# Performance work log

Measured on AMD Instinct MI355X. Metric: run time of the kernel, lower is better.

Reference implementation:

```python
import jax, jax.numpy as jnp
import numpy as np

B, S, D = 4, 2048, 768
H, R = 12, 8
Dh = D // H


def setup_inputs() -> dict:
    key = jax.random.key(0)
    ks = jax.random.split(key, 12)
    s_in = 1.0 / np.sqrt(D)
    s_r = 1.0 / np.sqrt(R)
    return {
        "x": jax.random.normal(ks[0], (B, S, D), jnp.float32),
        "Wq0": jax.random.normal(ks[1], (D, D), jnp.float32) * s_in,
        "Aq": jax.random.normal(ks[2], (D, R), jnp.float32) * s_in,
        "Bq": jax.random.normal(ks[3], (R, D), jnp.float32) * s_r,
        "Wk0": jax.random.normal(ks[4], (D, D), jnp.float32) * s_in,
        "Ak": jax.random.normal(ks[5], (D, R), jnp.float32) * s_in,
        "Bk": jax.random.normal(ks[6], (R, D), jnp.float32) * s_r,
        "Wv0": jax.random.normal(ks[7], (D, D), jnp.float32) * s_in,
        "Av": jax.random.normal(ks[8], (D, R), jnp.float32) * s_in,
        "Bv": jax.random.normal(ks[9], (R, D), jnp.float32) * s_r,
        "Wo": jax.random.normal(ks[10], (D, D), jnp.float32) * s_in,
        "bo": jnp.zeros((D,), jnp.float32),
    }


def _lora(x, W0, A, Bm):
    # x @ W0 + (x @ A) @ B  -- low-rank adapter on frozen W0
    return x @ W0 + (x @ A) @ Bm


def _split_heads(t):
    # [B,S,D] -> [B,H,S,Dh]
    return t.reshape(B, S, H, Dh).transpose(0, 2, 1, 3)


def reference(x, Wq0, Aq, Bq, Wk0, Ak, Bk, Wv0, Av, Bv, Wo, bo):
    q = _split_heads(_lora(x, Wq0, Aq, Bq))
    k = _split_heads(_lora(x, Wk0, Ak, Bk))
    v = _split_heads(_lora(x, Wv0, Av, Bv))
    scale = 1.0 / jnp.sqrt(jnp.asarray(Dh, x.dtype))
    scores = jnp.einsum("bhqd,bhkd->bhqk", q, k) * scale  # [B,H,S,S]
    weights = jax.nn.softmax(scores, axis=-1)
    attn = jnp.einsum("bhqk,bhkd->bhqd", weights, v)
    concat = attn.transpose(0, 2, 1, 3).reshape(B, S, D)
    return concat @ Wo + bo
```

## Files before the change

### kernel.cpp

```cpp
#include <hip/hip_runtime.h>
#include <hip/hip_bf16.h>


typedef unsigned short ushort_t;
typedef __bf16 bf16x8 __attribute__((ext_vector_type(8)));
typedef float f32x4 __attribute__((ext_vector_type(4)));
typedef float f32x16 __attribute__((ext_vector_type(16)));
typedef unsigned short ushort8 __attribute__((ext_vector_type(8)));
typedef unsigned short ushort4_t __attribute__((ext_vector_type(4)));
typedef unsigned int uint4v __attribute__((ext_vector_type(4)));
typedef __attribute__((address_space(1))) unsigned int gu32;
typedef __attribute__((address_space(3))) unsigned int lu32;

__device__ __forceinline__ unsigned short f2bf(float f) {
  unsigned int u = __builtin_bit_cast(unsigned int, f);
  u += 0x7fffu + ((u >> 16) & 1u);
  return (unsigned short)(u >> 16);
}

__device__ __forceinline__ void gld_lds16(const void* g, void* s) {
  __builtin_amdgcn_global_load_lds((gu32*)(unsigned long long)g,
                                   (lu32*)(unsigned int)(unsigned long long)s,
                                   16, 0, 0);
}

__device__ __forceinline__ f32x4 mfma16(bf16x8 a, bf16x8 b, f32x4 c) {
  return __builtin_amdgcn_mfma_f32_16x16x32_bf16(a, b, c, 0, 0, 0);
}

__device__ __forceinline__ f32x16 mfma32(bf16x8 a, bf16x8 b, f32x16 c) {
  return __builtin_amdgcn_mfma_f32_32x32x16_bf16(a, b, c, 0, 0, 0);
}

__device__ __forceinline__ unsigned int cvtpk(float a, float b) {
  unsigned int r;
  asm("v_cvt_pk_bf16_f32 %0, %1, %2" : "=v"(r) : "v"(a), "v"(b));
  return r;
}

__global__ __launch_bounds__(256) void prep_weights(
    const float* __restrict__ Wq0, const float* __restrict__ Aq, const float* __restrict__ Bq,
    const float* __restrict__ Wk0, const float* __restrict__ Ak, const float* __restrict__ Bk,
    const float* __restrict__ Wv0, const float* __restrict__ Av, const float* __restrict__ Bv,
    const float* __restrict__ Wo,
    ushort_t* __restrict__ WeffT, ushort_t* __restrict__ WoT)
{
  __shared__ float tile[32][33];
  __shared__ float tA[32][8];
  __shared__ float tB[8][32];
  const int mat = blockIdx.y;
  const int kt = blockIdx.x / 24, nt = blockIdx.x % 24;
  const int k0 = kt * 32, n0 = nt * 32;
  const float* W0 = (mat == 0) ? Wq0 : (mat == 1) ? Wk0 : (mat == 2) ? Wv0 : Wo;
  const float* Am = (mat == 0) ? Aq : (mat == 1) ? Ak : (mat == 2) ? Av : nullptr;
  const float* Bm = (mat == 0) ? Bq : (mat == 1) ? Bk : (mat == 2) ? Bv : nullptr;
  const int tid = threadIdx.x;
#pragma unroll
  for (int i = 0; i < 4; i++) {
    int rr = i * 8 + (tid >> 5), c = tid & 31;
    tile[rr][c] = W0[(k0 + rr) * 768 + n0 + c];
  }
  if (Am) {
    tA[tid >> 3][tid & 7] = Am[(k0 + (tid >> 3)) * 8 + (tid & 7)];
    tB[tid >> 5][tid & 31] = Bm[(tid >> 5) * 768 + n0 + (tid & 31)];
  }
  __syncthreads();
#pragma unroll
  for (int i = 0; i < 4; i++) {
    int kk = tid & 31;
    int nn = i * 8 + (tid >> 5);
    float val = tile[kk][nn];
    if (Am) {
#pragma unroll
      for (int rr = 0; rr < 8; rr++) val += tA[kk][rr] * tB[rr][nn];
    }
    int n = n0 + nn, kg = k0 + kk;
    if (mat < 3) WeffT[((long)mat * 768 + n) * 768 + kg] = f2bf(val);
    else         WoT[(long)n * 768 + kg] = f2bf(val);
  }
}

__global__ __launch_bounds__(256) void cast_x(const float* __restrict__ x,
                                              ushort_t* __restrict__ xb)
{
  long i = (long)blockIdx.x * 256 + threadIdx.x;
  const float4* xp = (const float4*)x;
  float4 a = xp[i * 2], c = xp[i * 2 + 1];
  ushort8 rv;
  rv[0] = f2bf(a.x); rv[1] = f2bf(a.y); rv[2] = f2bf(a.z); rv[3] = f2bf(a.w);
  rv[4] = f2bf(c.x); rv[5] = f2bf(c.y); rv[6] = f2bf(c.z); rv[7] = f2bf(c.w);
  *(ushort8*)&xb[i * 8] = rv;
}

template <int MODE>
__global__ __launch_bounds__(256) void gemm_bt(
    const ushort_t* __restrict__ A, const ushort_t* __restrict__ Bt,
    ushort_t* __restrict__ q, ushort_t* __restrict__ kbuf, ushort_t* __restrict__ vt,
    float* __restrict__ out, const float* __restrict__ bo)
{
  constexpr int K = 768;
  constexpr int NT = K / 64;
  __shared__ __align__(16) ushort_t As[2][128 * 64];
  __shared__ __align__(16) ushort_t Bs[2][128 * 64];
  const int tid = threadIdx.x;
  const int l = tid & 63, w = tid >> 6;
  const int wm = w >> 1, wn = w & 1;
  const int lr = l & 15, lg = l >> 4;
  const long rowBase = (long)blockIdx.x * 128;
  const long colBase = (long)blockIdx.y * 128;
  f32x4 acc[4][4] = {};

  int soff[4];
#pragma unroll
  for (int i = 0; i < 4; i++) {
    int ci = i * 256 + tid, r = ci >> 3, c = ci & 7;
    soff[i] = r * K + ((c ^ (r & 7)) * 8);
  }
  int rdoff[2];
#pragma unroll
  for (int ks = 0; ks < 2; ks++) rdoff[ks] = ((ks * 4 + lg) ^ (lr & 7)) * 8;

  const ushort_t* Abase = A + rowBase * K;
  const ushort_t* Bbase = Bt + colBase * K;

  auto STAGE = [&](int t, int bi) {
    const ushort_t* ap = Abase + t * 64;
    const ushort_t* bp = Bbase + t * 64;
#pragma unroll
    for (int i = 0; i < 4; i++)
      gld_lds16(ap + soff[i], &As[bi][(i * 256 + tid) * 8]);
#pragma unroll
    for (int i = 0; i < 4; i++)
      gld_lds16(bp + soff[i], &Bs[bi][(i * 256 + tid) * 8]);
  };

  STAGE(0, 0);

  for (int t = 0; t < NT; t++) {
    const int cur = t & 1;
    if (t + 1 < NT) {
      STAGE(t + 1, cur ^ 1);
      asm volatile("s_waitcnt vmcnt(8)" ::: "memory");
    } else {
      asm volatile("s_waitcnt vmcnt(0)" ::: "memory");
    }
    __builtin_amdgcn_s_barrier();
#pragma unroll
    for (int ks = 0; ks < 2; ks++) {
      bf16x8 af[4], bf[4];
#pragma unroll
      for (int m = 0; m < 4; m++)
        af[m] = *(const bf16x8*)&As[cur][(wm * 64 + m * 16 + lr) * 64 + rdoff[ks]];
#pragma unroll
      for (int n = 0; n < 4; n++)
        bf[n] = *(const bf16x8*)&Bs[cur][(wn * 64 + n * 16 + lr) * 64 + rdoff[ks]];
#pragma unroll
      for (int m = 0; m < 4; m++)
#pragma unroll
        for (int n = 0; n < 4; n++)
          acc[m][n] = mfma16(af[m], bf[n], acc[m][n]);
    }
    asm volatile("" ::: "memory");
    __builtin_amdgcn_s_barrier();
  }

  if (MODE == 0) {
    const int mat = (int)(colBase / 768);
    __syncthreads();
    ushort_t* myscr = (w < 2) ? &As[0][w * 4096] : &Bs[0][(w - 2) * 4096];
    if (mat == 2) {
      const long cb = colBase - 1536;
#pragma unroll
      for (int m = 0; m < 4; m++) {
        int sp0 = m * 16 + ((lg & 1) << 3) + ((lg >> 1) << 2);
#pragma unroll
        for (int n = 0; n < 4; n++) {
          int lcol = n * 16 + lr;
          int ch = (sp0 >> 3) ^ (lcol & 7);
          ushort4_t pk;
#pragma unroll
          for (int r = 0; r < 4; r++) pk[r] = f2bf(acc[m][n][r]);
          *(ushort4_t*)&myscr[lcol * 64 + ch * 8 + (sp0 & 7)] = pk;
        }
      }
      asm volatile("s_waitcnt lgkmcnt(0)" ::: "memory");
      const long sB = rowBase + wm * 64;
      const long bI = sB >> 11, sL = sB & 2047;
      const long cg = cb + wn * 64;
#pragma unroll
      for (int it = 0; it < 8; it++) {
        int cl = (l >> 3) + it * 8;
        int ch = (l & 7) ^ (cl & 7);
        ushort8 vv = *(const ushort8*)&myscr[cl * 64 + ch * 8];
        *(ushort8*)&vt[(bI * 768 + cg + cl) * 2048 + sL + (l & 7) * 8] = vv;
      }
    } else {
      ushort_t* dst = (mat == 0) ? q : kbuf;
      const float scl = (mat == 0) ? 0.125f * 1.4426950408889634f : 1.0f;
      const long cb = colBase - (long)mat * 768;
#pragma unroll
      for (int m = 0; m < 4; m++)
#pragma unroll
        for (int n = 0; n < 4; n++)
#pragma unroll
          for (int r = 0; r < 4; r++) {
            int lrow = m * 16 + lg * 4 + r, lcol = n * 16 + lr;
            int ch = (lcol >> 3) ^ (lrow & 7);
            myscr[lrow * 64 + ch * 8 + (lcol & 7)] = f2bf(acc[m][n][r] * scl);
          }
      asm volatile("s_waitcnt lgkmcnt(0)" ::: "memory");
      const long cg = cb + wn * 64;
#pragma unroll
      for (int it = 0; it < 8; it++) {
        int rl = (l >> 3) + it * 8;
        int ch = (l & 7) ^ (rl & 7);
        ushort8 vv = *(const ushort8*)&myscr[rl * 64 + ch * 8];
        *(ushort8*)&dst[(rowBase + wm * 64 + rl) * 768 + cg + (l & 7) * 8] = vv;
      }
    }
  } else {
#pragma unroll
    for (int m = 0; m < 4; m++)
#pragma unroll
      for (int n = 0; n < 4; n++) {
        long col = colBase + wn * 64 + n * 16 + lr;
        float bv = bo[col];
#pragma unroll
        for (int r = 0; r < 4; r++) {
          long row = rowBase + wm * 64 + m * 16 + lg * 4 + r;
          out[row * 768 + col] = acc[m][n][r] + bv;
        }
      }
  }
}

__global__ __launch_bounds__(256) void attn_fwd(
    const ushort_t* __restrict__ Q, const ushort_t* __restrict__ Kg,
    const ushort_t* __restrict__ VtG, ushort_t* __restrict__ O)
{
  constexpr int D = 768, S = 2048;
  __shared__ __align__(16) ushort_t Ks[2][64 * 64];
  __shared__ __align__(16) ushort_t Vs[2][64 * 64];
  const int tid = threadIdx.x;
  const int l = tid & 63, w = tid >> 6;
  const int q32 = l & 31, hi = l >> 5;
  const int i = blockIdx.x;
  const int xcd = i & 7, j = i >> 3;
  const int bh = xcd * 6 + (j >> 4);
  const int q0 = (j & 15) * 128;
  const int b = bh / 12, h = bh % 12;
  const ushort_t* Qb = Q + (long)b * S * D + h * 64;
  const ushort_t* Kb = Kg + (long)b * S * D + h * 64;
  const ushort_t* Vb = VtG + ((long)b * 768 + h * 64) * S;

  bf16x8 qf[4];
  {
    const ushort_t* qrow = Qb + (long)(q0 + w * 32 + q32) * D + hi * 8;
#pragma unroll
    for (int ks = 0; ks < 4; ks++) qf[ks] = *(const bf16x8*)&qrow[ks * 16];
  }

  int koff[2], voff[2];
#pragma unroll
  for (int it = 0; it < 2; it++) {
    int ci = it * 256 + tid, r = ci >> 3, c = ci & 7;
    koff[it] = r * D + ((c ^ (r & 7)) * 8);
    voff[it] = r * S + ((c ^ (r & 7)) * 8);
  }
  const int swz = q32 & 7;
  int rdoff[4];
#pragma unroll
  for (int ks = 0; ks < 4; ks++) rdoff[ks] = ((ks * 2 + hi) ^ swz) * 8;

  bf16x8 ones;
#pragma unroll
  for (int e = 0; e < 8; e++) ones[e] = (__bf16)1.0f;

  f32x16 oA = {}, oB = {}, osum = {};

  auto STAGE = [&](int kt, int bi) {
    const ushort_t* kp = Kb + (long)kt * 64 * D;
    const ushort_t* vp = Vb + kt * 64;
#pragma unroll
    for (int it = 0; it < 2; it++)
      gld_lds16(kp + koff[it], &Ks[bi][(it * 256 + tid) * 8]);
#pragma unroll
    for (int it = 0; it < 2; it++)
      gld_lds16(vp + voff[it], &Vs[bi][(it * 256 + tid) * 8]);
  };

  STAGE(0, 0);

  for (int kt = 0; kt < 32; kt++) {
    const int cur = kt & 1;
    STAGE((kt + 1) & 31, cur ^ 1);
    asm volatile("s_waitcnt vmcnt(4)" ::: "memory");
    __builtin_amdgcn_s_barrier();

    const ushort_t* ksb = &Ks[cur][0];
    const ushort_t* vsb = &Vs[cur][0];

    f32x16 s0 = {}, s1 = {};
    __builtin_amdgcn_s_setprio(1);
#pragma unroll
    for (int ks = 0; ks < 4; ks++) {
      bf16x8 kf0 = *(const bf16x8*)&ksb[q32 * 64 + rdoff[ks]];
      bf16x8 kf1 = *(const bf16x8*)&ksb[(32 + q32) * 64 + rdoff[ks]];
      s0 = mfma32(kf0, qf[ks], s0);
      s1 = mfma32(kf1, qf[ks], s1);
    }
    __builtin_amdgcn_s_setprio(0);

    unsigned int pw[16];
#pragma unroll
    for (int u = 0; u < 8; u++) {
      float a0 = __builtin_amdgcn_exp2f(s0[2 * u]);
      float a1 = __builtin_amdgcn_exp2f(s0[2 * u + 1]);
      pw[u] = cvtpk(a0, a1);
    }
#pragma unroll
    for (int u = 0; u < 8; u++) {
      float a0 = __builtin_amdgcn_exp2f(s1[2 * u]);
      float a1 = __builtin_amdgcn_exp2f(s1[2 * u + 1]);
      pw[8 + u] = cvtpk(a0, a1);
    }

    __builtin_amdgcn_s_setprio(1);
#pragma unroll
    for (int ks = 0; ks < 4; ks++) {
      uint4v w4 = {pw[4 * ks], pw[4 * ks + 1], pw[4 * ks + 2], pw[4 * ks + 3]};
      bf16x8 pa = __builtin_bit_cast(bf16x8, w4);
      bf16x8 vf0 = *(const bf16x8*)&vsb[q32 * 64 + rdoff[ks]];
      bf16x8 vf1 = *(const bf16x8*)&vsb[(32 + q32) * 64 + rdoff[ks]];
      oA = mfma32(pa, vf0, oA);
      oB = mfma32(pa, vf1, oB);
      osum = mfma32(pa, ones, osum);
    }
    __builtin_amdgcn_s_setprio(0);

    asm volatile("" ::: "memory");
    __builtin_amdgcn_s_barrier();
  }

#pragma unroll
  for (int reg = 0; reg < 16; reg++) {
    int row = (reg & 3) + 8 * (reg >> 2) + 4 * hi;
    float inv = 1.0f / osum[reg];
    long base = ((long)b * S + q0 + w * 32 + row) * D + h * 64 + q32;
    O[base] = f2bf(oA[reg] * inv);
    O[base + 32] = f2bf(oB[reg] * inv);
  }
}

extern "C" void kernel_launch(void* const* d_in, const int* in_sizes, int n_in,
                              void* d_out, int out_size, void* d_ws, size_t ws_size,
                              hipStream_t stream)
{
  const float* x   = (const float*)d_in[0];
  const float* Wq0 = (const float*)d_in[1];
  const float* Aq  = (const float*)d_in[2];
  const float* Bq  = (const float*)d_in[3];
  const float* Wk0 = (const float*)d_in[4];
  const float* Ak  = (const float*)d_in[5];
  const float* Bk  = (const float*)d_in[6];
  const float* Wv0 = (const float*)d_in[7];
  const float* Av  = (const float*)d_in[8];
  const float* Bv  = (const float*)d_in[9];
  const float* Wo  = (const float*)d_in[10];
  const float* bo  = (const float*)d_in[11];
  float* out = (float*)d_out;

  char* ws = (char*)d_ws;
  const long SZ = 8192L * 768 * 2;
  ushort_t* xb    = (ushort_t*)(ws);
  ushort_t* Qb    = (ushort_t*)(ws + SZ);
  ushort_t* Kb    = (ushort_t*)(ws + 2 * SZ);
  ushort_t* Vt    = (ushort_t*)(ws + 3 * SZ);
  ushort_t* At    = (ushort_t*)(ws + 4 * SZ);
  ushort_t* WeffT = (ushort_t*)(ws + 5 * SZ);
  ushort_t* WoT   = (ushort_t*)(ws + 5 * SZ + 2304L * 768 * 2);

  hipLaunchKernelGGL(prep_weights, dim3(576, 4), dim3(256), 0, stream,
                     Wq0, Aq, Bq, Wk0, Ak, Bk, Wv0, Av, Bv, Wo, WeffT, WoT);
  hipLaunchKernelGGL(cast_x, dim3(3072), dim3(256), 0, stream, x, xb);
  hipLaunchKernelGGL((gemm_bt<0>), dim3(64, 18), dim3(256), 0, stream,
                     xb, WeffT, Qb, Kb, Vt, (float*)nullptr, (const float*)nullptr);
  hipLaunchKernelGGL(attn_fwd, dim3(768), dim3(256), 0, stream, Qb, Kb, Vt, At);
  hipLaunchKernelGGL((gemm_bt<1>), dim3(64, 6), dim3(256), 0, stream,
                     At, WoT, (ushort_t*)nullptr, (ushort_t*)nullptr, (ushort_t*)nullptr,
                     out, bo);
}
```

Baseline: 153.1 us.

## Load attention K/V tiles directly into registers and merge prep with cast

The attention kernel no longer stages K and V tiles through double-buffered LDS with barriers. Each wave now loads its MFMA operand fragments straight from global memory into registers, prefetching the next tile after each use. Separately, the weight-prep and input-cast kernels are merged into one launch, saving a kernel launch. The register path removes LDS traffic and block barriers, but every wave fetches K/V independently, adding global/L2 traffic and exposing load latency with only one tile of lookahead.

Result: slower. 249.1 us (+62.7%).

```diff
diff --git a/kernel.cpp b/kernel.cpp
--- a/kernel.cpp
+++ b/kernel.cpp
@@ -38,23 +38,36 @@
   return r;
 }
 
-__global__ __launch_bounds__(256) void prep_weights(
+__global__ __launch_bounds__(256) void prep_and_cast(
+    const float* __restrict__ x,
     const float* __restrict__ Wq0, const float* __restrict__ Aq, const float* __restrict__ Bq,
     const float* __restrict__ Wk0, const float* __restrict__ Ak, const float* __restrict__ Bk,
     const float* __restrict__ Wv0, const float* __restrict__ Av, const float* __restrict__ Bv,
     const float* __restrict__ Wo,
-    ushort_t* __restrict__ WeffT, ushort_t* __restrict__ WoT)
+    ushort_t* __restrict__ xb, ushort_t* __restrict__ WeffT, ushort_t* __restrict__ WoT)
 {
+  const int tid = threadIdx.x;
+  const int bx = blockIdx.x;
+  if (bx < 3072) {
+    long i = (long)bx * 256 + tid;
+    const float4* xp = (const float4*)x;
+    float4 a = xp[i * 2], c = xp[i * 2 + 1];
+    ushort8 rv;
+    rv[0] = f2bf(a.x); rv[1] = f2bf(a.y); rv[2] = f2bf(a.z); rv[3] = f2bf(a.w);
+    rv[4] = f2bf(c.x); rv[5] = f2bf(c.y); rv[6] = f2bf(c.z); rv[7] = f2bf(c.w);
+    *(ushort8*)&xb[i * 8] = rv;
+    return;
+  }
   __shared__ float tile[32][33];
   __shared__ float tA[32][8];
   __shared__ float tB[8][32];
-  const int mat = blockIdx.y;
-  const int kt = blockIdx.x / 24, nt = blockIdx.x % 24;
+  const int bb = bx - 3072;
+  const int mat = bb / 576, inner = bb % 576;
+  const int kt = inner / 24, nt = inner % 24;
   const int k0 = kt * 32, n0 = nt * 32;
   const float* W0 = (mat == 0) ? Wq0 : (mat == 1) ? Wk0 : (mat == 2) ? Wv0 : Wo;
   const float* Am = (mat == 0) ? Aq : (mat == 1) ? Ak : (mat == 2) ? Av : nullptr;
   const float* Bm = (mat == 0) ? Bq : (mat == 1) ? Bk : (mat == 2) ? Bv : nullptr;
-  const int tid = threadIdx.x;
 #pragma unroll
   for (int i = 0; i < 4; i++) {
     int rr = i * 8 + (tid >> 5), c = tid & 31;
@@ -78,18 +91,6 @@
     if (mat < 3) WeffT[((long)mat * 768 + n) * 768 + kg] = f2bf(val);
     else         WoT[(long)n * 768 + kg] = f2bf(val);
   }
-}
-
-__global__ __launch_bounds__(256) void cast_x(const float* __restrict__ x,
-                                              ushort_t* __restrict__ xb)
-{
-  long i = (long)blockIdx.x * 256 + threadIdx.x;
-  const float4* xp = (const float4*)x;
-  float4 a = xp[i * 2], c = xp[i * 2 + 1];
-  ushort8 rv;
-  rv[0] = f2bf(a.x); rv[1] = f2bf(a.y); rv[2] = f2bf(a.z); rv[3] = f2bf(a.w);
-  rv[4] = f2bf(c.x); rv[5] = f2bf(c.y); rv[6] = f2bf(c.z); rv[7] = f2bf(c.w);
-  *(ushort8*)&xb[i * 8] = rv;
 }
 
 template <int MODE>
@@ -239,8 +240,6 @@
     const ushort_t* __restrict__ VtG, ushort_t* __restrict__ O)
 {
   constexpr int D = 768, S = 2048;
-  __shared__ __align__(16) ushort_t Ks[2][64 * 64];
-  __shared__ __align__(16) ushort_t Vs[2][64 * 64];
   const int tid = threadIdx.x;
   const int l = tid & 63, w = tid >> 6;
   const int q32 = l & 31, hi = l >> 5;
@@ -250,8 +249,11 @@
   const int q0 = (j & 15) * 128;
   const int b = bh / 12, h = bh % 12;
   const ushort_t* Qb = Q + (long)b * S * D + h * 64;
-  const ushort_t* Kb = Kg + (long)b * S * D + h * 64;
-  const ushort_t* Vb = VtG + ((long)b * 768 + h * 64) * S;
+
+  const ushort_t* kp0 = Kg + (long)b * S * D + h * 64 + (long)q32 * D + hi * 8;
+  const ushort_t* kp1 = kp0 + 32 * D;
+  const ushort_t* vp0 = VtG + ((long)b * 768 + h * 64 + q32) * S + hi * 8;
+  const ushort_t* vp1 = vp0 + 32 * S;
 
   bf16x8 qf[4];
   {
@@ -260,56 +262,39 @@
     for (int ks = 0; ks < 4; ks++) qf[ks] = *(const bf16x8*)&qrow[ks * 16];
   }
 
-  int koff[2], voff[2];
-#pragma unroll
-  for (int it = 0; it < 2; it++) {
-    int ci = it * 256 + tid, r = ci >> 3, c = ci & 7;
-    koff[it] = r * D + ((c ^ (r & 7)) * 8);
-    voff[it] = r * S + ((c ^ (r & 7)) * 8);
-  }
-  const int swz = q32 & 7;
-  int rdoff[4];
-#pragma unroll
-  for (int ks = 0; ks < 4; ks++) rdoff[ks] = ((ks * 2 + hi) ^ swz) * 8;
-
   bf16x8 ones;
 #pragma unroll
   for (int e = 0; e < 8; e++) ones[e] = (__bf16)1.0f;
 
   f32x16 oA = {}, oB = {}, osum = {};
 
-  auto STAGE = [&](int kt, int bi) {
-    const ushort_t* kp = Kb + (long)kt * 64 * D;
-    const ushort_t* vp = Vb + kt * 64;
-#pragma unroll
-    for (int it = 0; it < 2; it++)
-      gld_lds16(kp + koff[it], &Ks[bi][(it * 256 + tid) * 8]);
-#pragma unroll
-    for (int it = 0; it < 2; it++)
-      gld_lds16(vp + voff[it], &Vs[bi][(it * 256 + tid) * 8]);
-  };
-
-  STAGE(0, 0);
+  bf16x8 k0[4], k1[4], v0[4], v1[4];
+#pragma unroll
+  for (int ks = 0; ks < 4; ks++) {
+    k0[ks] = *(const bf16x8*)&kp0[ks * 16];
+    k1[ks] = *(const bf16x8*)&kp1[ks * 16];
+    v0[ks] = *(const bf16x8*)&vp0[ks * 16];
+    v1[ks] = *(const bf16x8*)&vp1[ks * 16];
+  }
+  kp0 += 64 * D; kp1 += 64 * D; vp0 += 64; vp1 += 64;
 
   for (int kt = 0; kt < 32; kt++) {
-    const int cur = kt & 1;
-    STAGE((kt + 1) & 31, cur ^ 1);
-    asm volatile("s_waitcnt vmcnt(4)" ::: "memory");
-    __builtin_amdgcn_s_barrier();
-
-    const ushort_t* ksb = &Ks[cur][0];
-    const ushort_t* vsb = &Vs[cur][0];
-
     f32x16 s0 = {}, s1 = {};
     __builtin_amdgcn_s_setprio(1);
 #pragma unroll
     for (int ks = 0; ks < 4; ks++) {
-      bf16x8 kf0 = *(const bf16x8*)&ksb[q32 * 64 + rdoff[ks]];
-      bf16x8 kf1 = *(const bf16x8*)&ksb[(32 + q32) * 64 + rdoff[ks]];
-      s0 = mfma32(kf0, qf[ks], s0);
-      s1 = mfma32(kf1, qf[ks], s1);
+      s0 = mfma32(k0[ks], qf[ks], s0);
+      s1 = mfma32(k1[ks], qf[ks], s1);
     }
     __builtin_amdgcn_s_setprio(0);
+    if (kt + 1 < 32) {
+#pragma unroll
+      for (int ks = 0; ks < 4; ks++) {
+        k0[ks] = *(const bf16x8*)&kp0[ks * 16];
+        k1[ks] = *(const bf16x8*)&kp1[ks * 16];
+      }
+      kp0 += 64 * D; kp1 += 64 * D;
+    }
 
     unsigned int pw[16];
 #pragma unroll
@@ -330,16 +315,19 @@
     for (int ks = 0; ks < 4; ks++) {
       uint4v w4 = {pw[4 * ks], pw[4 * ks + 1], pw[4 * ks + 2], pw[4 * ks + 3]};
       bf16x8 pa = __builtin_bit_cast(bf16x8, w4);
-      bf16x8 vf0 = *(const bf16x8*)&vsb[q32 * 64 + rdoff[ks]];
-      bf16x8 vf1 = *(const bf16x8*)&vsb[(32 + q32) * 64 + rdoff[ks]];
-      oA = mfma32(pa, vf0, oA);
-      oB = mfma32(pa, vf1, oB);
+      oA = mfma32(pa, v0[ks], oA);
+      oB = mfma32(pa, v1[ks], oB);
       osum = mfma32(pa, ones, osum);
     }
     __builtin_amdgcn_s_setprio(0);
-
-    asm volatile("" ::: "memory");
-    __builtin_amdgcn_s_barrier();
+    if (kt + 1 < 32) {
+#pragma unroll
+      for (int ks = 0; ks < 4; ks++) {
+        v0[ks] = *(const bf16x8*)&vp0[ks * 16];
+        v1[ks] = *(const bf16x8*)&vp1[ks * 16];
+      }
+      vp0 += 64; vp1 += 64;
+    }
   }
 
 #pragma unroll
@@ -380,9 +368,8 @@
   ushort_t* WeffT = (ushort_t*)(ws + 5 * SZ);
   ushort_t* WoT   = (ushort_t*)(ws + 5 * SZ + 2304L * 768 * 2);
 
-  hipLaunchKernelGGL(prep_weights, dim3(576, 4), dim3(256), 0, stream,
-                     Wq0, Aq, Bq, Wk0, Ak, Bk, Wv0, Av, Bv, Wo, WeffT, WoT);
-  hipLaunchKernelGGL(cast_x, dim3(3072), dim3(256), 0, stream, x, xb);
+  hipLaunchKernelGGL(prep_and_cast, dim3(3072 + 2304), dim3(256), 0, stream,
+                     x, Wq0, Aq, Bq, Wk0, Ak, Bk, Wv0, Av, Bv, Wo, xb, WeffT, WoT);
   hipLaunchKernelGGL((gemm_bt<0>), dim3(64, 18), dim3(256), 0, stream,
                      xb, WeffT, Qb, Kb, Vt, (float*)nullptr, (const float*)nullptr);
   hipLaunchKernelGGL(attn_fwd, dim3(768), dim3(256), 0, stream, Qb, Kb, Vt, At);
```
